# Performance work log

Hardware: AMD Instinct MI355X
Metric: run time of the kernel (lower is better)

Reference implementation:

```python
import jax, jax.numpy as jnp
import numpy as np

N_NODES = 50000


def gcn_conv(h, src, dst, W, b, n):
    # PyG GCNConv: x' = D^{-1/2} (A + I) D^{-1/2} (h W) + b
    x = h @ W  # [N, out]
    deg = jax.ops.segment_sum(jnp.ones_like(src, dtype=x.dtype), dst, num_segments=n) + 1.0  # self-loop
    dis = deg ** -0.5
    norm = dis[src] * dis[dst]  # [E]
    msg = x[src] * norm[:, None]  # [E, out]
    agg = jax.ops.segment_sum(msg, dst, num_segments=n)
    agg = agg + x * (dis * dis)[:, None]  # self-loop term: 1/deg_i * x_i
    return agg + b


def setup_inputs() -> dict:
    key = jax.random.key(0)
    ks = jax.random.split(key, 8)
    n, e = N_NODES, 800000
    d_in, d_rni, h = 128, 32, 256
    x = jax.random.normal(ks[0], (n, d_in), dtype=jnp.float32)
    rni = jax.random.normal(ks[1], (n, d_rni), dtype=jnp.float32)
    edge_index = jax.random.randint(ks[2], (2, e), 0, n, dtype=jnp.int64)
    s1 = (d_in + d_rni) ** -0.5
    s2 = h ** -0.5
    W1 = jax.random.normal(ks[3], (d_in + d_rni, h), dtype=jnp.float32) * s1
    b1 = jnp.zeros((h,), dtype=jnp.float32)
    W2 = jax.random.normal(ks[4], (h, h), dtype=jnp.float32) * s2
    b2 = jnp.zeros((h,), dtype=jnp.float32)
    W_out = jax.random.normal(ks[5], (h, h), dtype=jnp.float32) * s2
    b_out = jnp.zeros((h,), dtype=jnp.float32)
    return {"x": x, "rni": rni, "edge_index": edge_index, "W1": W1, "b1": b1,
            "W2": W2, "b2": b2, "W_out": W_out, "b_out": b_out}


def reference(x, rni, edge_index, W1, b1, W2, b2, W_out, b_out):
    n = x.shape[0]
    src, dst = edge_index[0], edge_index[1]
    h = jnp.concatenate([x, rni], axis=-1)  # RNI concat
    h = jax.nn.relu(gcn_conv(h, src, dst, W1, b1, n))
    h = jax.nn.relu(gcn_conv(h, src, dst, W2, b2, n))
    return h @ W_out + b_out
```

## Files before the change

kernel.cpp:

```cpp
#include <hip/hip_runtime.h>
#include <hip/hip_bf16.h>
#include <hip/hip_fp16.h>
#include <math.h>

#define D_IN   128
#define D_RNI  32
#define HID    256
#define NCHUNK 8

typedef _Float16 half8 __attribute__((ext_vector_type(8)));
typedef float    f32x4 __attribute__((ext_vector_type(4)));

__global__ void k_detect_zero(const unsigned int* __restrict__ w, int nwords,
                              int* __restrict__ mode, int* __restrict__ counts, int n) {
    int i = blockIdx.x * 256 + threadIdx.x;
    if (i < n) counts[i] = 0;
    if (blockIdx.x == 0) {
        __shared__ unsigned int red[256];
        unsigned int acc = 0;
        for (int j = threadIdx.x; j < 1024; j += 256) {
            int idx = 2 * j + 1;
            if (idx < nwords) acc |= w[idx];
        }
        red[threadIdx.x] = acc;
        __syncthreads();
        for (int s = 128; s > 0; s >>= 1) {
            if (threadIdx.x < s) red[threadIdx.x] |= red[threadIdx.x + s];
            __syncthreads();
        }
        if (threadIdx.x == 0) *mode = (red[0] == 0u) ? 1 : 0;
    }
}

__global__ void k_count(const unsigned int* __restrict__ ew, const int* __restrict__ mode_p,
                        int* __restrict__ counts, int e) {
    int mode = *mode_p;
    int i = blockIdx.x * 256 + threadIdx.x;
    if (i >= e) return;
    int d = mode ? (int)ew[2 * ((size_t)e + i)] : (int)ew[(size_t)e + i];
    atomicAdd(&counts[d], 1);
}

__global__ __launch_bounds__(1024) void k_scan1(const int* __restrict__ counts,
                                                int* __restrict__ incl,
                                                int* __restrict__ bsum, int n) {
    __shared__ int sd[1024];
    int t = threadIdx.x;
    int i = blockIdx.x * 1024 + t;
    int v = (i < n) ? counts[i] : 0;
    sd[t] = v;
    __syncthreads();
    for (int off = 1; off < 1024; off <<= 1) {
        int tmp = (t >= off) ? sd[t - off] : 0;
        __syncthreads();
        sd[t] += tmp;
        __syncthreads();
    }
    if (i < n) incl[i] = sd[t];
    if (t == 1023) bsum[blockIdx.x] = sd[1023];
}

__global__ __launch_bounds__(1024) void k_scan2(int* __restrict__ bsum, int nb) {
    __shared__ int sd[1024];
    int t = threadIdx.x;
    int v = (t < nb) ? bsum[t] : 0;
    sd[t] = v;
    __syncthreads();
    for (int off = 1; off < 1024; off <<= 1) {
        int tmp = (t >= off) ? sd[t - off] : 0;
        __syncthreads();
        sd[t] += tmp;
        __syncthreads();
    }
    if (t < nb) bsum[t] = sd[t] - v;
    if (t == nb - 1) bsum[nb] = sd[t];
}

__global__ void k_scan3(const int* __restrict__ counts, const int* __restrict__ incl,
                        const int* __restrict__ bsum,
                        int* __restrict__ rowptr, int* __restrict__ cursor,
                        float* __restrict__ dis, int n, int nb) {
    int i = blockIdx.x * 256 + threadIdx.x;
    if (i >= n) return;
    int excl = incl[i] - counts[i] + bsum[i >> 10];
    rowptr[i] = excl;
    cursor[i] = excl;
    dis[i] = 1.0f / sqrtf((float)(counts[i] + 1));
    if (i == 0) rowptr[n] = bsum[nb];
}

__global__ void k_scatter(const unsigned int* __restrict__ ew, const int* __restrict__ mode_p,
                          int* __restrict__ cursor, const float* __restrict__ dis,
                          uint2* __restrict__ csrw, int e) {
    int mode = *mode_p;
    int i = blockIdx.x * 256 + threadIdx.x;
    if (i >= e) return;
    int s, d;
    if (mode) {
        s = (int)ew[2 * (size_t)i];
        d = (int)ew[2 * ((size_t)e + i)];
    } else {
        s = (int)ew[(size_t)i];
        d = (int)ew[(size_t)e + i];
    }
    float w = dis[s] * dis[d];
    int pos = atomicAdd(&cursor[d], 1);
    uint2 m;
    m.x = (unsigned int)s;
    m.y = __float_as_uint(w);
    csrw[pos] = m;
}

#define TW1 (160 * 256)
#define TW2 (256 * 256)
__global__ void k_cvt_all(const float* __restrict__ W1, const float* __restrict__ W2,
                          const float* __restrict__ Wo,
                          __half* __restrict__ W1t, __half* __restrict__ W2t,
                          __half* __restrict__ Wot) {
    int i = blockIdx.x * 256 + threadIdx.x;
    if (i < TW1) {
        int k = i / 256, nn = i & 255;
        W1t[(size_t)nn * 160 + k] = __float2half(W1[i]);
    } else if (i < TW1 + TW2) {
        int j = i - TW1;
        int k = j >> 8, nn = j & 255;
        W2t[(size_t)nn * 256 + k] = __float2half(W2[j]);
    } else if (i < TW1 + 2 * TW2) {
        int j = i - TW1 - TW2;
        int k = j >> 8, nn = j & 255;
        Wot[(size_t)nn * 256 + k] = __float2half(Wo[j]);
    }
}

#define KT 32
#define LSTR 40
template <bool A_F32, bool ADD_BIAS, bool HALF_OUT>
__global__ __launch_bounds__(256) void k_mgemm(const void* __restrict__ Av, int strideA, int KA,
                                               const void* __restrict__ A2v, int strideA2,
                                               const __half* __restrict__ Bt,
                                               const float* __restrict__ bias,
                                               void* Cv, int M, int K) {
    __shared__ __half As[64 * LSTR];
    __shared__ __half Bs[256 * LSTR];
    int tid = threadIdx.x;
    int wave = tid >> 6, lane = tid & 63;
    int q = lane >> 4, m16 = lane & 15;
    int r0 = blockIdx.x * 64;

    f32x4 acc[4][4] = {};

    for (int k0 = 0; k0 < K; k0 += KT) {
        __syncthreads();
        {
            int r = tid >> 2, kq = (tid & 3) * 8;
            int row = r0 + r; if (row >= M) row = M - 1;
            if (A_F32) {
                const float* src; int stride, kk0;
                if (k0 < KA) { src = (const float*)Av;  stride = strideA;  kk0 = k0; }
                else         { src = (const float*)A2v; stride = strideA2; kk0 = k0 - KA; }
                const float* p = &src[(size_t)row * stride + kk0 + kq];
                float4 va = *reinterpret_cast<const float4*>(p);
                float4 vb = *reinterpret_cast<const float4*>(p + 4);
                union { __half2 h2[4]; uint4 u; } uu;
                uu.h2[0] = __floats2half2_rn(va.x, va.y);
                uu.h2[1] = __floats2half2_rn(va.z, va.w);
                uu.h2[2] = __floats2half2_rn(vb.x, vb.y);
                uu.h2[3] = __floats2half2_rn(vb.z, vb.w);
                *reinterpret_cast<uint4*>(&As[r * LSTR + kq]) = uu.u;
            } else {
                const __half* src = (const __half*)Av;
                uint4 v = *reinterpret_cast<const uint4*>(&src[(size_t)row * strideA + k0 + kq]);
                *reinterpret_cast<uint4*>(&As[r * LSTR + kq]) = v;
            }
        }
        {
            int nb = tid >> 2, kq = (tid & 3) * 8;
            #pragma unroll
            for (int i = 0; i < 4; ++i) {
                int nn = nb + i * 64;
                uint4 v = *reinterpret_cast<const uint4*>(&Bt[(size_t)nn * K + k0 + kq]);
                *reinterpret_cast<uint4*>(&Bs[nn * LSTR + kq]) = v;
            }
        }
        __syncthreads();

        half8 af[4], bf[4];
        #pragma unroll
        for (int mi = 0; mi < 4; ++mi)
            af[mi] = *reinterpret_cast<const half8*>(&As[(mi * 16 + m16) * LSTR + q * 8]);
        #pragma unroll
        for (int ni = 0; ni < 4; ++ni)
            bf[ni] = *reinterpret_cast<const half8*>(&Bs[(wave * 64 + ni * 16 + m16) * LSTR + q * 8]);
        #pragma unroll
        for (int mi = 0; mi < 4; ++mi)
            #pragma unroll
            for (int ni = 0; ni < 4; ++ni)
                acc[mi][ni] = __builtin_amdgcn_mfma_f32_16x16x32_f16(af[mi], bf[ni], acc[mi][ni], 0, 0, 0);
    }

    #pragma unroll
    for (int mi = 0; mi < 4; ++mi) {
        #pragma unroll
        for (int r = 0; r < 4; ++r) {
            int row = r0 + mi * 16 + q * 4 + r;
            if (row >= M) continue;
            #pragma unroll
            for (int ni = 0; ni < 4; ++ni) {
                int col = wave * 64 + ni * 16 + m16;
                float v = acc[mi][ni][r];
                if (ADD_BIAS) v += bias[col];
                if (HALF_OUT) {
                    size_t addr = ((size_t)(col >> 5) * M + row) * 32 + (col & 31);
                    ((__half*)Cv)[addr] = __float2half(v);
                } else {
                    ((float*)Cv)[(size_t)row * HID + col] = v;
                }
            }
        }
    }
}

__global__ __launch_bounds__(256) void k_agg(const __half* __restrict__ xh,
                                             const int* __restrict__ rowptr,
                                             const uint2* __restrict__ csrw,
                                             const float* __restrict__ dis,
                                             const float* __restrict__ bias,
                                             __half* __restrict__ outh, int n) {
    int chunk = blockIdx.x & 7;
    int g     = blockIdx.x >> 3;
    int sub   = threadIdx.x >> 3;
    int cpos  = threadIdx.x & 7;
    int i = g * 32 + sub;
    if (i >= n) return;

    const __half* base = xh + (size_t)chunk * n * 32;
    float disd = dis[i];
    int e0 = rowptr[i], e1 = rowptr[i + 1];

    float a0, a1, a2, a3;
    {
        uint2 sv = *reinterpret_cast<const uint2*>(&base[(size_t)i * 32 + cpos * 4]);
        float2 f0 = __half22float2(*reinterpret_cast<__half2*>(&sv.x));
        float2 f1 = __half22float2(*reinterpret_cast<__half2*>(&sv.y));
        float ws = disd * disd;
        a0 = f0.x * ws; a1 = f0.y * ws; a2 = f1.x * ws; a3 = f1.y * ws;
    }

    int ee = e0;
    for (; ee + 4 <= e1; ee += 4) {
        uint2 m0 = csrw[ee + 0];
        uint2 m1 = csrw[ee + 1];
        uint2 m2 = csrw[ee + 2];
        uint2 m3 = csrw[ee + 3];
        uint2 v0 = *reinterpret_cast<const uint2*>(&base[(size_t)m0.x * 32 + cpos * 4]);
        uint2 v1 = *reinterpret_cast<const uint2*>(&base[(size_t)m1.x * 32 + cpos * 4]);
        uint2 v2 = *reinterpret_cast<const uint2*>(&base[(size_t)m2.x * 32 + cpos * 4]);
        uint2 v3 = *reinterpret_cast<const uint2*>(&base[(size_t)m3.x * 32 + cpos * 4]);
        float w0 = __uint_as_float(m0.y), w1 = __uint_as_float(m1.y);
        float w2 = __uint_as_float(m2.y), w3 = __uint_as_float(m3.y);
        float2 p0 = __half22float2(*reinterpret_cast<__half2*>(&v0.x));
        float2 q0 = __half22float2(*reinterpret_cast<__half2*>(&v0.y));
        float2 p1 = __half22float2(*reinterpret_cast<__half2*>(&v1.x));
        float2 q1 = __half22float2(*reinterpret_cast<__half2*>(&v1.y));
        float2 p2 = __half22float2(*reinterpret_cast<__half2*>(&v2.x));
        float2 q2 = __half22float2(*reinterpret_cast<__half2*>(&v2.y));
        float2 p3 = __half22float2(*reinterpret_cast<__half2*>(&v3.x));
        float2 q3 = __half22float2(*reinterpret_cast<__half2*>(&v3.y));
        a0 = fmaf(p0.x, w0, a0); a1 = fmaf(p0.y, w0, a1);
        a2 = fmaf(q0.x, w0, a2); a3 = fmaf(q0.y, w0, a3);
        a0 = fmaf(p1.x, w1, a0); a1 = fmaf(p1.y, w1, a1);
        a2 = fmaf(q1.x, w1, a2); a3 = fmaf(q1.y, w1, a3);
        a0 = fmaf(p2.x, w2, a0); a1 = fmaf(p2.y, w2, a1);
        a2 = fmaf(q2.x, w2, a2); a3 = fmaf(q2.y, w2, a3);
        a0 = fmaf(p3.x, w3, a0); a1 = fmaf(p3.y, w3, a1);
        a2 = fmaf(q3.x, w3, a2); a3 = fmaf(q3.y, w3, a3);
    }
    for (; ee < e1; ++ee) {
        uint2 m = csrw[ee];
        float w = __uint_as_float(m.y);
        uint2 v = *reinterpret_cast<const uint2*>(&base[(size_t)m.x * 32 + cpos * 4]);
        float2 p = __half22float2(*reinterpret_cast<__half2*>(&v.x));
        float2 q = __half22float2(*reinterpret_cast<__half2*>(&v.y));
        a0 = fmaf(p.x, w, a0); a1 = fmaf(p.y, w, a1);
        a2 = fmaf(q.x, w, a2); a3 = fmaf(q.y, w, a3);
    }

    int cbase = chunk * 32 + cpos * 4;
    float4 bb = *reinterpret_cast<const float4*>(&bias[cbase]);
    union { __half2 h2[2]; uint2 u; } o;
    o.h2[0] = __floats2half2_rn(fmaxf(a0 + bb.x, 0.0f), fmaxf(a1 + bb.y, 0.0f));
    o.h2[1] = __floats2half2_rn(fmaxf(a2 + bb.z, 0.0f), fmaxf(a3 + bb.w, 0.0f));
    *reinterpret_cast<uint2*>(&outh[(size_t)i * HID + cbase]) = o.u;
}

extern "C" void kernel_launch(void* const* d_in, const int* in_sizes, int n_in,
                              void* d_out, int out_size, void* d_ws, size_t ws_size,
                              hipStream_t stream) {
    const float* x     = (const float*)d_in[0];
    const float* rni   = (const float*)d_in[1];
    const unsigned int* ew = (const unsigned int*)d_in[2];
    const float* W1    = (const float*)d_in[3];
    const float* b1    = (const float*)d_in[4];
    const float* W2    = (const float*)d_in[5];
    const float* b2    = (const float*)d_in[6];
    const float* W_out = (const float*)d_in[7];
    const float* b_out = (const float*)d_in[8];
    float* out = (float*)d_out;

    const int n  = in_sizes[0] / D_IN;
    const int e  = in_sizes[2] / 2;
    const int nb = (n + 1023) / 1024;
    const int K1 = D_IN + D_RNI;

    char* ws = (char*)d_ws;
    size_t off = 0;
    auto carve = [&](size_t bytes) {
        char* p = ws + off;
        off = (off + bytes + 255) & ~(size_t)255;
        return p;
    };
    __half* xh    = (__half*)carve((size_t)n * HID * sizeof(__half));
    __half* h     = (__half*)carve((size_t)n * HID * sizeof(__half));
    __half* W1t   = (__half*)carve((size_t)K1 * HID * sizeof(__half));
    __half* W2t   = (__half*)carve((size_t)HID * HID * sizeof(__half));
    __half* Wot   = (__half*)carve((size_t)HID * HID * sizeof(__half));
    int*   counts = (int*)carve((size_t)n * sizeof(int));
    int*   incl   = (int*)carve((size_t)n * sizeof(int));
    int*   bsum   = (int*)carve((size_t)(nb + 1) * sizeof(int));
    int*   rowptr = (int*)carve((size_t)(n + 1) * sizeof(int));
    int*   cursor = (int*)carve((size_t)n * sizeof(int));
    float* dis    = (float*)carve((size_t)n * sizeof(float));
    uint2* csrw   = (uint2*)carve((size_t)e * sizeof(uint2));
    int*   mode   = (int*)carve(sizeof(int));
    (void)ws_size;

    const int eb = (e + 255) / 256;
    const int gemm_blocks = (n + 63) / 64;
    const int agg_blocks  = NCHUNK * ((n + 31) / 32);

    k_detect_zero<<<(n + 255) / 256, 256, 0, stream>>>(ew, 2 * e, mode, counts, n);
    k_count<<<eb, 256, 0, stream>>>(ew, mode, counts, e);
    k_scan1<<<nb, 1024, 0, stream>>>(counts, incl, bsum, n);
    k_scan2<<<1, 1024, 0, stream>>>(bsum, nb);
    k_scan3<<<(n + 255) / 256, 256, 0, stream>>>(counts, incl, bsum, rowptr, cursor, dis, n, nb);
    k_scatter<<<eb, 256, 0, stream>>>(ew, mode, cursor, dis, csrw, e);

    {
        int tot = TW1 + 2 * TW2;
        k_cvt_all<<<(tot + 255) / 256, 256, 0, stream>>>(W1, W2, W_out, W1t, W2t, Wot);
    }

    k_mgemm<true, false, true><<<gemm_blocks, 256, 0, stream>>>(x, D_IN, D_IN, rni, D_RNI,
                                                                W1t, nullptr, xh, n, K1);
    k_agg<<<agg_blocks, 256, 0, stream>>>(xh, rowptr, csrw, dis, b1, h, n);

    k_mgemm<false, false, true><<<gemm_blocks, 256, 0, stream>>>(h, HID, HID, nullptr, 0,
                                                                 W2t, nullptr, xh, n, HID);
    k_agg<<<agg_blocks, 256, 0, stream>>>(xh, rowptr, csrw, dis, b2, h, n);

    k_mgemm<false, true, false><<<gemm_blocks, 256, 0, stream>>>(h, HID, HID, nullptr, 0,
                                                                 Wot, b_out, out, n, HID);
}
```

Before: 394.1 us.

## Sort nodes by degree for aggregation and software-pipeline 8-wide edge gathers

Builds a degree histogram and a counting-sort permutation so each aggregation wavefront processes nodes of similar in-degree, which reduces divergence from uneven row lengths. The edge loop is rewritten to fetch 8 neighbor rows at a time with padded dummy entries and to prefetch the next batch of CSR entries while the current gathers are in flight. This adds two small kernels plus atomics, and gives up the natural node ordering of the aggregation, which may hurt locality of the output writes and of the self-row reads.

```diff
diff --git a/kernel.cpp b/kernel.cpp
--- a/kernel.cpp
+++ b/kernel.cpp
@@ -12,9 +12,11 @@
 typedef float    f32x4 __attribute__((ext_vector_type(4)));
 
 __global__ void k_detect_zero(const unsigned int* __restrict__ w, int nwords,
-                              int* __restrict__ mode, int* __restrict__ counts, int n) {
+                              int* __restrict__ mode, int* __restrict__ counts,
+                              int* __restrict__ dhist, int n) {
     int i = blockIdx.x * 256 + threadIdx.x;
     if (i < n) counts[i] = 0;
+    if (i < 64) dhist[i] = 0;
     if (blockIdx.x == 0) {
         __shared__ unsigned int red[256];
         unsigned int acc = 0;
@@ -79,14 +81,32 @@
 __global__ void k_scan3(const int* __restrict__ counts, const int* __restrict__ incl,
                         const int* __restrict__ bsum,
                         int* __restrict__ rowptr, int* __restrict__ cursor,
-                        float* __restrict__ dis, int n, int nb) {
+                        float* __restrict__ dis, int* __restrict__ dhist, int n, int nb) {
     int i = blockIdx.x * 256 + threadIdx.x;
     if (i >= n) return;
-    int excl = incl[i] - counts[i] + bsum[i >> 10];
+    int c = counts[i];
+    int excl = incl[i] - c + bsum[i >> 10];
     rowptr[i] = excl;
     cursor[i] = excl;
-    dis[i] = 1.0f / sqrtf((float)(counts[i] + 1));
+    dis[i] = 1.0f / sqrtf((float)(c + 1));
+    atomicAdd(&dhist[c > 63 ? 63 : c], 1);
     if (i == 0) rowptr[n] = bsum[nb];
+}
+
+__global__ void k_order1(const int* __restrict__ dhist, int* __restrict__ dcur) {
+    if (threadIdx.x == 0 && blockIdx.x == 0) {
+        int acc = 0;
+        for (int d = 0; d < 64; ++d) { int c = dhist[d]; dcur[d] = acc; acc += c; }
+    }
+}
+
+__global__ void k_order2(const int* __restrict__ counts, int* __restrict__ dcur,
+                         int* __restrict__ order, int n) {
+    int i = blockIdx.x * 256 + threadIdx.x;
+    if (i >= n) return;
+    int d = counts[i]; if (d > 63) d = 63;
+    int p = atomicAdd(&dcur[d], 1);
+    order[p] = i;
 }
 
 __global__ void k_scatter(const unsigned int* __restrict__ ew, const int* __restrict__ mode_p,
@@ -223,6 +243,7 @@
 __global__ __launch_bounds__(256) void k_agg(const __half* __restrict__ xh,
                                              const int* __restrict__ rowptr,
                                              const uint2* __restrict__ csrw,
+                                             const int* __restrict__ order,
                                              const float* __restrict__ dis,
                                              const float* __restrict__ bias,
                                              __half* __restrict__ outh, int n) {
@@ -230,12 +251,14 @@
     int g     = blockIdx.x >> 3;
     int sub   = threadIdx.x >> 3;
     int cpos  = threadIdx.x & 7;
-    int i = g * 32 + sub;
-    if (i >= n) return;
+    int slot = g * 32 + sub;
+    if (slot >= n) return;
+    int i = order[slot];
 
     const __half* base = xh + (size_t)chunk * n * 32;
     float disd = dis[i];
     int e0 = rowptr[i], e1 = rowptr[i + 1];
+    int nb8 = (e1 - e0 + 7) >> 3;
 
     float a0, a1, a2, a3;
     {
@@ -246,43 +269,37 @@
         a0 = f0.x * ws; a1 = f0.y * ws; a2 = f1.x * ws; a3 = f1.y * ws;
     }
 
-    int ee = e0;
-    for (; ee + 4 <= e1; ee += 4) {
-        uint2 m0 = csrw[ee + 0];
-        uint2 m1 = csrw[ee + 1];
-        uint2 m2 = csrw[ee + 2];
-        uint2 m3 = csrw[ee + 3];
-        uint2 v0 = *reinterpret_cast<const uint2*>(&base[(size_t)m0.x * 32 + cpos * 4]);
-        uint2 v1 = *reinterpret_cast<const uint2*>(&base[(size_t)m1.x * 32 + cpos * 4]);
-        uint2 v2 = *reinterpret_cast<const uint2*>(&base[(size_t)m2.x * 32 + cpos * 4]);
-        uint2 v3 = *reinterpret_cast<const uint2*>(&base[(size_t)m3.x * 32 + cpos * 4]);
-        float w0 = __uint_as_float(m0.y), w1 = __uint_as_float(m1.y);
-        float w2 = __uint_as_float(m2.y), w3 = __uint_as_float(m3.y);
-        float2 p0 = __half22float2(*reinterpret_cast<__half2*>(&v0.x));
-        float2 q0 = __half22float2(*reinterpret_cast<__half2*>(&v0.y));
-        float2 p1 = __half22float2(*reinterpret_cast<__half2*>(&v1.x));
-        float2 q1 = __half22float2(*reinterpret_cast<__half2*>(&v1.y));
-        float2 p2 = __half22float2(*reinterpret_cast<__half2*>(&v2.x));
-        float2 q2 = __half22float2(*reinterpret_cast<__half2*>(&v2.y));
-        float2 p3 = __half22float2(*reinterpret_cast<__half2*>(&v3.x));
-        float2 q3 = __half22float2(*reinterpret_cast<__half2*>(&v3.y));
-        a0 = fmaf(p0.x, w0, a0); a1 = fmaf(p0.y, w0, a1);
-        a2 = fmaf(q0.x, w0, a2); a3 = fmaf(q0.y, w0, a3);
-        a0 = fmaf(p1.x, w1, a0); a1 = fmaf(p1.y, w1, a1);
-        a2 = fmaf(q1.x, w1, a2); a3 = fmaf(q1.y, w1, a3);
-        a0 = fmaf(p2.x, w2, a0); a1 = fmaf(p2.y, w2, a1);
-        a2 = fmaf(q2.x, w2, a2); a3 = fmaf(q2.y, w2, a3);
-        a0 = fmaf(p3.x, w3, a0); a1 = fmaf(p3.y, w3, a1);
-        a2 = fmaf(q3.x, w3, a2); a3 = fmaf(q3.y, w3, a3);
-    }
-    for (; ee < e1; ++ee) {
-        uint2 m = csrw[ee];
-        float w = __uint_as_float(m.y);
-        uint2 v = *reinterpret_cast<const uint2*>(&base[(size_t)m.x * 32 + cpos * 4]);
-        float2 p = __half22float2(*reinterpret_cast<__half2*>(&v.x));
-        float2 q = __half22float2(*reinterpret_cast<__half2*>(&v.y));
-        a0 = fmaf(p.x, w, a0); a1 = fmaf(p.y, w, a1);
-        a2 = fmaf(q.x, w, a2); a3 = fmaf(q.y, w, a3);
+    uint2 m[8];
+    #pragma unroll
+    for (int u = 0; u < 8; ++u) {
+        int ee = e0 + u;
+        if (ee < e1) m[u] = csrw[ee];
+        else { m[u].x = (unsigned int)i; m[u].y = 0u; }
+    }
+    int eb = e0 + 8;
+    for (int b = 0; b < nb8; ++b) {
+        uint2 v[8];
+        #pragma unroll
+        for (int u = 0; u < 8; ++u)
+            v[u] = *reinterpret_cast<const uint2*>(&base[(size_t)m[u].x * 32 + cpos * 4]);
+        uint2 mn[8];
+        #pragma unroll
+        for (int u = 0; u < 8; ++u) {
+            int ee = eb + u;
+            if (ee < e1) mn[u] = csrw[ee];
+            else { mn[u].x = (unsigned int)i; mn[u].y = 0u; }
+        }
+        eb += 8;
+        #pragma unroll
+        for (int u = 0; u < 8; ++u) {
+            float w = __uint_as_float(m[u].y);
+            float2 p = __half22float2(*reinterpret_cast<__half2*>(&v[u].x));
+            float2 q = __half22float2(*reinterpret_cast<__half2*>(&v[u].y));
+            a0 = fmaf(p.x, w, a0); a1 = fmaf(p.y, w, a1);
+            a2 = fmaf(q.x, w, a2); a3 = fmaf(q.y, w, a3);
+        }
+        #pragma unroll
+        for (int u = 0; u < 8; ++u) m[u] = mn[u];
     }
 
     int cbase = chunk * 32 + cpos * 4;
@@ -331,6 +348,9 @@
     int*   cursor = (int*)carve((size_t)n * sizeof(int));
     float* dis    = (float*)carve((size_t)n * sizeof(float));
     uint2* csrw   = (uint2*)carve((size_t)e * sizeof(uint2));
+    int*   dhist  = (int*)carve(64 * sizeof(int));
+    int*   dcur   = (int*)carve(64 * sizeof(int));
+    int*   order  = (int*)carve((size_t)n * sizeof(int));
     int*   mode   = (int*)carve(sizeof(int));
     (void)ws_size;
 
@@ -338,11 +358,13 @@
     const int gemm_blocks = (n + 63) / 64;
     const int agg_blocks  = NCHUNK * ((n + 31) / 32);
 
-    k_detect_zero<<<(n + 255) / 256, 256, 0, stream>>>(ew, 2 * e, mode, counts, n);
+    k_detect_zero<<<(n + 255) / 256, 256, 0, stream>>>(ew, 2 * e, mode, counts, dhist, n);
     k_count<<<eb, 256, 0, stream>>>(ew, mode, counts, e);
     k_scan1<<<nb, 1024, 0, stream>>>(counts, incl, bsum, n);
     k_scan2<<<1, 1024, 0, stream>>>(bsum, nb);
-    k_scan3<<<(n + 255) / 256, 256, 0, stream>>>(counts, incl, bsum, rowptr, cursor, dis, n, nb);
+    k_scan3<<<(n + 255) / 256, 256, 0, stream>>>(counts, incl, bsum, rowptr, cursor, dis, dhist, n, nb);
+    k_order1<<<1, 64, 0, stream>>>(dhist, dcur);
+    k_order2<<<(n + 255) / 256, 256, 0, stream>>>(counts, dcur, order, n);
     k_scatter<<<eb, 256, 0, stream>>>(ew, mode, cursor, dis, csrw, e);
 
     {
@@ -352,11 +374,11 @@
 
     k_mgemm<true, false, true><<<gemm_blocks, 256, 0, stream>>>(x, D_IN, D_IN, rni, D_RNI,
                                                                 W1t, nullptr, xh, n, K1);
-    k_agg<<<agg_blocks, 256, 0, stream>>>(xh, rowptr, csrw, dis, b1, h, n);
+    k_agg<<<agg_blocks, 256, 0, stream>>>(xh, rowptr, csrw, order, dis, b1, h, n);
 
     k_mgemm<false, false, true><<<gemm_blocks, 256, 0, stream>>>(h, HID, HID, nullptr, 0,
                                                                  W2t, nullptr, xh, n, HID);
-    k_agg<<<agg_blocks, 256, 0, stream>>>(xh, rowptr, csrw, dis, b2, h, n);
+    k_agg<<<agg_blocks, 256, 0, stream>>>(xh, rowptr, csrw, order, dis, b2, h, n);
 
     k_mgemm<false, true, false><<<gemm_blocks, 256, 0, stream>>>(h, HID, HID, nullptr, 0,
                                                                  Wot, b_out, out, n, HID);
```

New measurement: 684.9 us. 1.74x slower.
